# Kernel optimization log

Hardware: AMD Instinct MI355X
Metric: run time of the kernel (lower is better)

## Reference

```python
import jax, jax.numpy as jnp
import numpy as np

B, S, D_IN, D_FF, D_OUT, E = 4, 2048, 1024, 4096, 1024, 8


def setup_inputs() -> dict:
    key = jax.random.key(0)
    ks = jax.random.split(key, 8)
    s = lambda k, shape, fan: jax.random.normal(k, shape, dtype=jnp.float32) * (1.0 / np.sqrt(fan))
    return {
        "x": jax.random.normal(ks[0], (B, S, D_IN), dtype=jnp.float32),
        "switch_w": s(ks[1], (D_IN, E), D_IN),
        "switch_b": jnp.zeros((E,), dtype=jnp.float32),
        "w1": s(ks[2], (E, D_IN, D_FF), D_IN),
        "b1": jnp.zeros((E, D_FF), dtype=jnp.float32),
        "w2": s(ks[3], (E, D_FF, D_OUT), D_FF),
        "b2": jnp.zeros((E, D_OUT), dtype=jnp.float32),
    }


def reference(x, switch_w, switch_b, w1, b1, w2, b2):
    b, s, d = x.shape
    n_experts = w1.shape[0]
    xf = x.reshape(-1, d)                                   # [T, d]
    route_prob = jax.nn.softmax(xf @ switch_w + switch_b, axis=-1)  # [T, E]
    route_prob_max = jnp.max(route_prob, axis=-1)           # [T]
    routes = jnp.argmax(route_prob, axis=-1)                # [T] int, constant wrt grads

    # Per-expert FFN applied to all tokens, combined with top-1 one-hot mask
    # (drop_tokens=False -> every token goes to exactly its argmax expert).
    h = jax.nn.relu(jnp.einsum('td,edf->etf', xf, w1) + b1[:, None, :])   # [E, T, f]
    y_all = jnp.einsum('etf,efo->eto', h, w2) + b2[:, None, :]            # [E, T, d_out]
    onehot = jax.nn.one_hot(routes, n_experts, dtype=xf.dtype)            # [T, E]
    y = jnp.einsum('eto,te->to', y_all, onehot)             # dispatch-combine

    # is_scale_prob=True: scale output by routing probability
    y = y * route_prob_max[:, None]

    counts = onehot.sum(axis=0)                             # tokens per expert
    route_frac = counts / counts.sum()
    aux_loss = n_experts * jnp.sum(route_frac * route_prob.sum(axis=0))

    return y.reshape(b, s, -1), aux_loss
```

## Files before the change

### kernel.cpp

```cpp
#include <hip/hip_runtime.h>
#include <cstdint>
#include <cstddef>

#define NT   8192
#define DIN  1024
#define DFF  4096
#define DOUT 1024
#define NEXP 8

typedef float  f32x4v __attribute__((ext_vector_type(4)));
typedef short  s16x8  __attribute__((ext_vector_type(8)));
typedef short  s16x4  __attribute__((ext_vector_type(4)));

__device__ __forceinline__ ushort f2bf(float f) {
  union { float f; uint32_t u; } c; c.f = f;
  uint32_t u = c.u;
  return (ushort)((u + 0x7fffu + ((u >> 16) & 1u)) >> 16);
}

__global__ __launch_bounds__(256) void router_kernel(
    const float* __restrict__ x, const float* __restrict__ sw,
    const float* __restrict__ sb,
    int* __restrict__ routes, int* __restrict__ posArr,
    float* __restrict__ pmaxArr,
    int* __restrict__ cnt, float* __restrict__ probsum) {
  __shared__ int   sRoute[64];
  __shared__ float sProb[4][NEXP];
  __shared__ int   sBase[NEXP];

  const int lane = threadIdx.x & 63;
  const int w    = threadIdx.x >> 6;
  const int t0   = blockIdx.x * 64;

  float bias[NEXP];
#pragma unroll
  for (int e = 0; e < NEXP; e++) bias[e] = sb[e];

  float wprob[NEXP];
#pragma unroll
  for (int e = 0; e < NEXP; e++) wprob[e] = 0.0f;

  for (int k = 0; k < 16; k++) {
    const int t = t0 + w * 16 + k;
    const float* xr = x + (size_t)t * DIN;
    float acc[NEXP];
#pragma unroll
    for (int e = 0; e < NEXP; e++) acc[e] = 0.0f;
#pragma unroll
    for (int it = 0; it < DIN / 64; it++) {
      const int i = it * 64 + lane;
      const float xv = xr[i];
      const float4 s0 = *(const float4*)(sw + (size_t)i * NEXP);
      const float4 s1 = *(const float4*)(sw + (size_t)i * NEXP + 4);
      acc[0] += xv * s0.x; acc[1] += xv * s0.y; acc[2] += xv * s0.z; acc[3] += xv * s0.w;
      acc[4] += xv * s1.x; acc[5] += xv * s1.y; acc[6] += xv * s1.z; acc[7] += xv * s1.w;
    }
#pragma unroll
    for (int e = 0; e < NEXP; e++) {
#pragma unroll
      for (int off = 32; off > 0; off >>= 1) acc[e] += __shfl_xor(acc[e], off, 64);
    }
    float m = acc[0] + bias[0]; int am = 0;
    float lg[NEXP];
#pragma unroll
    for (int e = 0; e < NEXP; e++) {
      lg[e] = acc[e] + bias[e];
      if (lg[e] > m) { m = lg[e]; am = e; }
    }
    float esum = 0.0f;
    float pe[NEXP];
#pragma unroll
    for (int e = 0; e < NEXP; e++) { pe[e] = __expf(lg[e] - m); esum += pe[e]; }
    const float inv = 1.0f / esum;
#pragma unroll
    for (int e = 0; e < NEXP; e++) wprob[e] += pe[e] * inv;
    if (lane == 0) {
      routes[t] = am;
      pmaxArr[t] = inv;
      sRoute[w * 16 + k] = am;
    }
  }
  if (lane == 0) {
#pragma unroll
    for (int e = 0; e < NEXP; e++) sProb[w][e] = wprob[e];
  }
  __syncthreads();

  const int tid = threadIdx.x;
  if (tid < NEXP) {
    float s = sProb[0][tid] + sProb[1][tid] + sProb[2][tid] + sProb[3][tid];
    atomicAdd(&probsum[tid], s);
    int c = 0;
#pragma unroll
    for (int j = 0; j < 64; j++) c += (sRoute[j] == tid);
    sBase[tid] = atomicAdd(&cnt[tid], c);
  }
  __syncthreads();

  if (tid < 64) {
    const int r = sRoute[tid];
    int rank = 0;
    for (int j = 0; j < 64; j++) rank += (j < tid) & (sRoute[j] == r);
    posArr[t0 + tid] = sBase[r] + rank;
  }
}

__global__ void offsets_aux_kernel(const int* __restrict__ cnt, const float* __restrict__ probsum,
                                   int* __restrict__ offsets, float* __restrict__ auxout) {
  if (threadIdx.x == 0) {
    int o = 0; float aux = 0.0f;
    for (int e = 0; e < NEXP; e++) {
      offsets[e] = o; o += cnt[e];
      aux += (float)cnt[e] * probsum[e];
    }
    offsets[NEXP] = o;
    auxout[0] = aux * ((float)NEXP / (float)NT);
  }
}

__global__ void gather_kernel(const float* __restrict__ x, const int* __restrict__ routes,
                              const int* __restrict__ posArr, const int* __restrict__ offsets,
                              int* __restrict__ perm, ushort* __restrict__ Xg) {
  const int lane = threadIdx.x & 63;
  const int t = (blockIdx.x * blockDim.x + threadIdx.x) >> 6;
  if (t >= NT) return;
  const int slot = offsets[routes[t]] + posArr[t];
  if (lane == 0) perm[slot] = t;
  const float* src = x + (size_t)t * DIN;
  ushort* dst = Xg + (size_t)slot * DIN;
#pragma unroll
  for (int half = 0; half < 2; half++) {
    int i = half * 512 + lane * 8;
    float4 v0 = *(const float4*)(src + i);
    float4 v1 = *(const float4*)(src + i + 4);
    s16x8 p;
    p[0] = (short)f2bf(v0.x); p[1] = (short)f2bf(v0.y);
    p[2] = (short)f2bf(v0.z); p[3] = (short)f2bf(v0.w);
    p[4] = (short)f2bf(v1.x); p[5] = (short)f2bf(v1.y);
    p[6] = (short)f2bf(v1.z); p[7] = (short)f2bf(v1.w);
    *(s16x8*)(dst + i) = p;
  }
}

__global__ void transpose_cvt_kernel(const float* __restrict__ src, ushort* __restrict__ dst,
                                     const int K, const int N) {
  __shared__ float tile[64][65];
  const int ntn = N >> 6;
  const int ntk = K >> 6;
  int b = blockIdx.x;
  const int tn = b % ntn; b /= ntn;
  const int tk = b % ntk; const int e = b / ntk;
  const float* s = src + ((size_t)e * K + (size_t)tk * 64) * N + (size_t)tn * 64;
  const int c4 = (threadIdx.x & 15) * 4;
  const int r0 = threadIdx.x >> 4;
#pragma unroll
  for (int p = 0; p < 4; p++) {
    const int row = r0 + p * 16;
    float4 v = *(const float4*)(s + (size_t)row * N + c4);
    tile[row][c4 + 0] = v.x; tile[row][c4 + 1] = v.y;
    tile[row][c4 + 2] = v.z; tile[row][c4 + 3] = v.w;
  }
  __syncthreads();
  ushort* d = dst + ((size_t)e * N + (size_t)tn * 64) * K + (size_t)tk * 64;
#pragma unroll
  for (int p = 0; p < 4; p++) {
    const int nrow = r0 + p * 16;
    s16x4 o;
    o[0] = (short)f2bf(tile[c4 + 0][nrow]);
    o[1] = (short)f2bf(tile[c4 + 1][nrow]);
    o[2] = (short)f2bf(tile[c4 + 2][nrow]);
    o[3] = (short)f2bf(tile[c4 + 3][nrow]);
    *(s16x4*)(d + (size_t)nrow * K + c4) = o;
  }
}

#define GLD16(g, l)                                                                        \
  __builtin_amdgcn_global_load_lds((const __attribute__((address_space(1))) uint32_t*)(g), \
                                   (__attribute__((address_space(3))) uint32_t*)(l), 16, 0, 0)

#define SBAR()   asm volatile("s_barrier" ::: "memory")
#define WAITV(n) asm volatile("s_waitcnt vmcnt(" #n ")" ::: "memory")
#define LGKM0()  asm volatile("s_waitcnt lgkmcnt(0)" ::: "memory")

template <int KDIM, int EPI>
__global__ __launch_bounds__(512, 1) void moe_gemm8p_kernel(
    const ushort* __restrict__ A,
    const ushort* __restrict__ BT,
    const float* __restrict__ bias,
    const int* __restrict__ offsets,
    ushort* __restrict__ Hout,
    float* __restrict__ Y,
    const int* __restrict__ perm, const float* __restrict__ pmaxArr,
    const int N) {
  __shared__ ushort sA4[4][8192];
  __shared__ ushort sB4[4][8192];
  int e, bx, by;
  if constexpr (EPI == 0) {
    const int logical = ((blockIdx.x & 7) << 7) + (blockIdx.x >> 3);
    e = logical >> 7;
    bx = (logical & 127) >> 3;
    by = logical & 7;
  } else {
    bx = blockIdx.x; by = blockIdx.y; e = blockIdx.z;
  }
  const int mlimit = offsets[e + 1];
  const int m0 = offsets[e] + by * 256;
  if (m0 >= mlimit) return;
  const int n0 = bx * 256;
  const int tid = threadIdx.x;
  const int lane = tid & 63;
  const int wid = tid >> 6;
  const int wr = wid >> 2;
  const int wc = wid & 3;
  const int hb = wc >> 1;
  const int rsel = lane & 15;
  const int lhi = lane >> 4;

  const int srow = wid * 8 + (lane >> 3);
  const int scol = ((lane & 7) ^ (lane >> 3)) * 8;
  const ushort* gA = A + (size_t)(m0 + srow) * KDIM + scol;
  const ushort* gB = BT + ((size_t)e * N + n0 + srow) * KDIM + scol;
  const int ldst = tid * 8;
  const size_t LK = (size_t)KDIM;

#define STAGE_A(s, h, kt)                                              \
  do {                                                                 \
    const ushort* g_ = gA + (size_t)((h) * 128) * LK + (size_t)(kt) * 64; \
    GLD16(g_, &sA4[s][ldst]);                                          \
    GLD16(g_ + 64 * LK, &sA4[s][ldst + 4096]);                         \
  } while (0)
#define STAGE_B(s, h, kt)                                              \
  do {                                                                 \
    const ushort* g_ = gB + (size_t)((h) * 128) * LK + (size_t)(kt) * 64; \
    GLD16(g_, &sB4[s][ldst]);                                          \
    GLD16(g_ + 64 * LK, &sB4[s][ldst + 4096]);                         \
  } while (0)

  f32x4v acc[2][4][4];
#pragma unroll
  for (int g = 0; g < 2; g++)
#pragma unroll
    for (int mf = 0; mf < 4; mf++)
#pragma unroll
      for (int nf = 0; nf < 4; nf++) acc[g][mf][nf] = (f32x4v)0.0f;

  const int rsw = rsel & 7;
  const int sw0 = ((lhi) ^ rsw) * 8;
  const int sw1 = ((4 + lhi) ^ rsw) * 8;
  const int arow0 = rsel * 64;
  const int brow0 = ((wc & 1) * 64 + rsel) * 64;

  s16x8 a[4][2], b0[2][2], b1[2][2];

#define LDA03(slot)                                                    \
  do {                                                                 \
    _Pragma("unroll") for (int mf = 0; mf < 4; mf++) {                 \
      a[mf][0] = *(const s16x8*)&sA4[slot][arow0 + mf * 1024 + sw0];   \
      a[mf][1] = *(const s16x8*)&sA4[slot][arow0 + mf * 1024 + sw1];   \
    }                                                                  \
  } while (0)
#define LDA47(slot)                                                    \
  do {                                                                 \
    _Pragma("unroll") for (int mf = 0; mf < 4; mf++) {                 \
      a[mf][0] = *(const s16x8*)&sA4[slot][arow0 + 4096 + mf * 1024 + sw0]; \
      a[mf][1] = *(const s16x8*)&sA4[slot][arow0 + 4096 + mf * 1024 + sw1]; \
    }                                                                  \
  } while (0)
#define LDB2(dst, slot, nfb)                                           \
  do {                                                                 \
    _Pragma("unroll") for (int nf = 0; nf < 2; nf++) {                 \
      dst[nf][0] = *(const s16x8*)&sB4[slot][brow0 + ((nfb) + nf) * 1024 + sw0]; \
      dst[nf][1] = *(const s16x8*)&sB4[slot][brow0 + ((nfb) + nf) * 1024 + sw1]; \
    }                                                                  \
  } while (0)
#define MFMAPH(MG, BB, NFB)                                            \
  do {                                                                 \
    __builtin_amdgcn_s_setprio(1);                                     \
    _Pragma("unroll") for (int mf = 0; mf < 4; mf++)                   \
    _Pragma("unroll") for (int nf = 0; nf < 2; nf++)                   \
    _Pragma("unroll") for (int ks = 0; ks < 2; ks++)                   \
      acc[MG][mf][(NFB) + nf] = __builtin_amdgcn_mfma_f32_16x16x32_bf16( \
          a[mf][ks], BB[nf][ks], acc[MG][mf][(NFB) + nf], 0, 0, 0);    \
    __builtin_amdgcn_s_setprio(0);                                     \
  } while (0)

  constexpr int NS = KDIM / 64;
  STAGE_A(0, 0, 0); STAGE_A(1, 1, 0); STAGE_B(0, 0, 0); STAGE_B(1, 1, 0);
  STAGE_B(2, 0, 1); STAGE_B(3, 1, 1); STAGE_A(2, 0, 1); STAGE_A(3, 1, 1);
  WAITV(8);
  SBAR();

#pragma unroll 2
  for (int t = 0; t < NS; ++t) {
    const int sa = (2 * t + wr) & 3;
    const int sb = (2 * t + hb) & 3;
    const int r0s = (2 * t) & 3, r1s = (2 * t + 1) & 3;
    const bool st2 = (t + 2 < NS);
    LDA03(sa);
    LDB2(b0, sb, 0);
    LDB2(b1, sb, 2);
    LGKM0(); SBAR();
    MFMAPH(0, b0, 0);
    LDA47(sa);
    LGKM0(); SBAR();
    MFMAPH(0, b1, 2);
    if (st2) { STAGE_B(r0s, 0, t + 2); STAGE_B(r1s, 1, t + 2); }
    SBAR();
    MFMAPH(1, b1, 2);
    if (st2) { STAGE_A(r0s, 0, t + 2); STAGE_A(r1s, 1, t + 2); }
    if (st2) { WAITV(8); } else { WAITV(0); }
    SBAR();
    MFMAPH(1, b0, 0);
  }
#undef LDA03
#undef LDA47
#undef LDB2
#undef MFMAPH
#undef STAGE_A
#undef STAGE_B

  float bv[4];
#pragma unroll
  for (int nf = 0; nf < 4; nf++)
    bv[nf] = bias[(size_t)e * N + n0 + wc * 64 + nf * 16 + rsel];
#pragma unroll
  for (int mg = 0; mg < 2; mg++) {
#pragma unroll
    for (int mf = 0; mf < 4; mf++) {
#pragma unroll
      for (int r = 0; r < 4; r++) {
        const int grow = m0 + wr * 128 + mg * 64 + mf * 16 + lhi * 4 + r;
        if (grow < mlimit) {
          if constexpr (EPI == 0) {
            ushort* hrow = Hout + (size_t)grow * N + n0 + wc * 64;
#pragma unroll
            for (int nf = 0; nf < 4; nf++) {
              float v = acc[mg][mf][nf][r] + bv[nf];
              hrow[nf * 16 + rsel] = f2bf(fmaxf(v, 0.0f));
            }
          } else {
            const int tok = perm[grow];
            const float sc = pmaxArr[tok];
            float* yrow = Y + (size_t)tok * N + n0 + wc * 64;
#pragma unroll
            for (int nf = 0; nf < 4; nf++)
              yrow[nf * 16 + rsel] = (acc[mg][mf][nf][r] + bv[nf]) * sc;
          }
        }
      }
    }
  }
}

extern "C" void kernel_launch(void* const* d_in, const int* in_sizes, int n_in,
                              void* d_out, int out_size, void* d_ws, size_t ws_size,
                              hipStream_t stream) {
  const float* x  = (const float*)d_in[0];
  const float* sw = (const float*)d_in[1];
  const float* sb = (const float*)d_in[2];
  const float* w1 = (const float*)d_in[3];
  const float* b1 = (const float*)d_in[4];
  const float* w2 = (const float*)d_in[5];
  const float* b2 = (const float*)d_in[6];
  float* out = (float*)d_out;
  float* auxp = out + (size_t)NT * DOUT;

  char* wsb = (char*)d_ws;
  int*   cnt      = (int*)wsb;
  float* probsum  = (float*)(wsb + 32);
  int*   offsets  = (int*)(wsb + 64);
  int*   routes   = (int*)(wsb + 256);
  int*   posArr   = routes + NT;
  float* pmaxArr  = (float*)(posArr + NT);
  int*   perm     = (int*)(pmaxArr + NT);
  ushort* Xg = (ushort*)(wsb + 256 + (size_t)4 * 4 * NT);
  ushort* Hg = Xg + (size_t)(NT + 256) * DIN;
  ushort* Wt = Hg + (size_t)(NT + 256) * DFF;
  size_t needed = (size_t)((char*)Wt - wsb) + (size_t)NEXP * DFF * DIN * 2;
  if (ws_size < needed) return;

  hipMemsetAsync(d_ws, 0, 64, stream);

  router_kernel<<<NT / 64, 256, 0, stream>>>(x, sw, sb, routes, posArr, pmaxArr, cnt, probsum);
  offsets_aux_kernel<<<1, 64, 0, stream>>>(cnt, probsum, offsets, auxp);
  gather_kernel<<<NT / 4, 256, 0, stream>>>(x, routes, posArr, offsets, perm, Xg);

  transpose_cvt_kernel<<<NEXP * (DIN / 64) * (DFF / 64), 256, 0, stream>>>(w1, Wt, DIN, DFF);
  moe_gemm8p_kernel<DIN, 0><<<1024, 512, 0, stream>>>(
      Xg, Wt, b1, offsets, Hg, nullptr, nullptr, nullptr, DFF);

  transpose_cvt_kernel<<<NEXP * (DFF / 64) * (DOUT / 64), 256, 0, stream>>>(w2, Wt, DFF, DOUT);
  moe_gemm8p_kernel<DFF, 1><<<dim3(DOUT / 256, 8, NEXP), 512, 0, stream>>>(
      Hg, Wt, b2, offsets, nullptr, out, perm, pmaxArr, DOUT);
}
```

Baseline: 358.0 us.

## Split-K the second MoE GEMM into two halves with a combine kernel

The second expert GEMM (K=4096) is split into two K halves across a doubled grid z dimension. Part 0 writes the scaled result directly to the output, and part 1 writes bf16 partials into reused workspace. A new combine kernel then adds the scaled partials into the output. The aim is more blocks and better CU occupancy for the small-N second GEMM, at the cost of an extra kernel, extra memory traffic and bf16 rounding of one partial. The grid y is also raised to 10 and barriers in the main loop are reordered to overlap B staging earlier.

```diff
diff --git a/kernel.cpp b/kernel.cpp
--- a/kernel.cpp
+++ b/kernel.cpp
@@ -16,6 +16,9 @@
   union { float f; uint32_t u; } c; c.f = f;
   uint32_t u = c.u;
   return (ushort)((u + 0x7fffu + ((u >> 16) & 1u)) >> 16);
+}
+__device__ __forceinline__ float bf2f(ushort h) {
+  union { uint32_t u; float f; } c; c.u = ((uint32_t)h) << 16; return c.f;
 }
 
 __global__ __launch_bounds__(256) void router_kernel(
@@ -190,19 +193,23 @@
     const int* __restrict__ offsets,
     ushort* __restrict__ Hout,
     float* __restrict__ Y,
+    ushort* __restrict__ P1,
     const int* __restrict__ perm, const float* __restrict__ pmaxArr,
-    const int N) {
+    const int N, const int LDK) {
   __shared__ ushort sA4[4][8192];
   __shared__ ushort sB4[4][8192];
-  int e, bx, by;
+  int e, bx, by, part;
   if constexpr (EPI == 0) {
     const int logical = ((blockIdx.x & 7) << 7) + (blockIdx.x >> 3);
     e = logical >> 7;
     bx = (logical & 127) >> 3;
     by = logical & 7;
+    part = 0;
   } else {
-    bx = blockIdx.x; by = blockIdx.y; e = blockIdx.z;
-  }
+    bx = blockIdx.x; by = blockIdx.y;
+    e = blockIdx.z & 7; part = blockIdx.z >> 3;
+  }
+  const size_t kofs = (size_t)part * KDIM;
   const int mlimit = offsets[e + 1];
   const int m0 = offsets[e] + by * 256;
   if (m0 >= mlimit) return;
@@ -218,10 +225,10 @@
 
   const int srow = wid * 8 + (lane >> 3);
   const int scol = ((lane & 7) ^ (lane >> 3)) * 8;
-  const ushort* gA = A + (size_t)(m0 + srow) * KDIM + scol;
-  const ushort* gB = BT + ((size_t)e * N + n0 + srow) * KDIM + scol;
+  const ushort* gA = A + (size_t)(m0 + srow) * LDK + kofs + scol;
+  const ushort* gB = BT + ((size_t)e * N + n0 + srow) * LDK + kofs + scol;
   const int ldst = tid * 8;
-  const size_t LK = (size_t)KDIM;
+  const size_t LK = (size_t)LDK;
 
 #define STAGE_A(s, h, kt)                                              \
   do {                                                                 \
@@ -301,11 +308,11 @@
     LDB2(b1, sb, 2);
     LGKM0(); SBAR();
     MFMAPH(0, b0, 0);
+    SBAR();
+    MFMAPH(0, b1, 2);
     LDA47(sa);
+    if (st2) { STAGE_B(r0s, 0, t + 2); STAGE_B(r1s, 1, t + 2); }
     LGKM0(); SBAR();
-    MFMAPH(0, b1, 2);
-    if (st2) { STAGE_B(r0s, 0, t + 2); STAGE_B(r1s, 1, t + 2); }
-    SBAR();
     MFMAPH(1, b1, 2);
     if (st2) { STAGE_A(r0s, 0, t + 2); STAGE_A(r1s, 1, t + 2); }
     if (st2) { WAITV(8); } else { WAITV(0); }
@@ -339,16 +346,48 @@
               hrow[nf * 16 + rsel] = f2bf(fmaxf(v, 0.0f));
             }
           } else {
-            const int tok = perm[grow];
-            const float sc = pmaxArr[tok];
-            float* yrow = Y + (size_t)tok * N + n0 + wc * 64;
-#pragma unroll
-            for (int nf = 0; nf < 4; nf++)
-              yrow[nf * 16 + rsel] = (acc[mg][mf][nf][r] + bv[nf]) * sc;
+            if (part == 0) {
+              const int tok = perm[grow];
+              const float sc = pmaxArr[tok];
+              float* yrow = Y + (size_t)tok * N + n0 + wc * 64;
+#pragma unroll
+              for (int nf = 0; nf < 4; nf++)
+                yrow[nf * 16 + rsel] = (acc[mg][mf][nf][r] + bv[nf]) * sc;
+            } else {
+              ushort* prow = P1 + (size_t)grow * N + n0 + wc * 64;
+#pragma unroll
+              for (int nf = 0; nf < 4; nf++)
+                prow[nf * 16 + rsel] = f2bf(acc[mg][mf][nf][r]);
+            }
           }
         }
       }
     }
+  }
+}
+
+__global__ __launch_bounds__(256) void combine_kernel(
+    const ushort* __restrict__ P1, const int* __restrict__ perm,
+    const float* __restrict__ pmaxArr, float* __restrict__ out) {
+  const int lane = threadIdx.x & 63;
+  const int slot = (blockIdx.x * blockDim.x + threadIdx.x) >> 6;
+  if (slot >= NT) return;
+  const int tok = perm[slot];
+  const float sc = pmaxArr[tok];
+  const ushort* src = P1 + (size_t)slot * DOUT;
+  float* dst = out + (size_t)tok * DOUT;
+#pragma unroll
+  for (int half = 0; half < 2; half++) {
+    const int i = half * 512 + lane * 8;
+    const s16x8 p = *(const s16x8*)(src + i);
+    float4 o0 = *(const float4*)(dst + i);
+    float4 o1 = *(const float4*)(dst + i + 4);
+    o0.x += sc * bf2f((ushort)p[0]); o0.y += sc * bf2f((ushort)p[1]);
+    o0.z += sc * bf2f((ushort)p[2]); o0.w += sc * bf2f((ushort)p[3]);
+    o1.x += sc * bf2f((ushort)p[4]); o1.y += sc * bf2f((ushort)p[5]);
+    o1.z += sc * bf2f((ushort)p[6]); o1.w += sc * bf2f((ushort)p[7]);
+    *(float4*)(dst + i) = o0;
+    *(float4*)(dst + i + 4) = o1;
   }
 }
 
@@ -378,6 +417,7 @@
   ushort* Wt = Hg + (size_t)(NT + 256) * DFF;
   size_t needed = (size_t)((char*)Wt - wsb) + (size_t)NEXP * DFF * DIN * 2;
   if (ws_size < needed) return;
+  ushort* P1 = Xg;
 
   hipMemsetAsync(d_ws, 0, 64, stream);
 
@@ -387,9 +427,10 @@
 
   transpose_cvt_kernel<<<NEXP * (DIN / 64) * (DFF / 64), 256, 0, stream>>>(w1, Wt, DIN, DFF);
   moe_gemm8p_kernel<DIN, 0><<<1024, 512, 0, stream>>>(
-      Xg, Wt, b1, offsets, Hg, nullptr, nullptr, nullptr, DFF);
+      Xg, Wt, b1, offsets, Hg, nullptr, nullptr, nullptr, nullptr, DFF, DIN);
 
   transpose_cvt_kernel<<<NEXP * (DFF / 64) * (DOUT / 64), 256, 0, stream>>>(w2, Wt, DFF, DOUT);
-  moe_gemm8p_kernel<DFF, 1><<<dim3(DOUT / 256, 8, NEXP), 512, 0, stream>>>(
-      Hg, Wt, b2, offsets, nullptr, out, perm, pmaxArr, DOUT);
-}
+  moe_gemm8p_kernel<DFF / 2, 3><<<dim3(DOUT / 256, 10, 16), 512, 0, stream>>>(
+      Hg, Wt, b2, offsets, nullptr, out, P1, perm, pmaxArr, DOUT, DFF);
+  combine_kernel<<<NT / 4, 256, 0, stream>>>(P1, perm, pmaxArr, out);
+}
```

Measured after the change: 387.5 us. 8.2% more time.
